# Kernel optimization log

Measured on AMD Instinct MI355X. Metric: run time of the kernel, lower is better.

The kernel has to match this reference:

```python
import jax, jax.numpy as jnp
import numpy as np

B, C, X, Y, Z = 2, 4, 128, 128, 96
_BIG = 1e10  # effectively infinite squared distance (no background in line)


def _edt_sq_pass(f, axis):
    """One separable pass of the exact squared EDT along `axis`:
    g[i] = min_j f[j] + (i - j)^2  (Felzenszwalb lower envelope, brute-forced
    with lax.map so only O(rest) memory per step)."""
    f = jnp.moveaxis(f, axis, -1)  # (..., L)
    idx = jnp.arange(f.shape[-1], dtype=f.dtype)
    g = jax.lax.map(lambda i: jnp.min(f + (i - idx) ** 2, axis=-1), idx)  # (L, ...)
    return jnp.moveaxis(jnp.moveaxis(g, 0, -1), -1, axis)


def _edt(mask):
    """Exact Euclidean distance of True voxels to the nearest False voxel
    (matches scipy.ndimage.distance_transform_edt on a binary mask)."""
    f = jnp.where(mask, _BIG, 0.0).astype(jnp.float32)
    for ax in (-3, -2, -1):  # three spatial axes
        f = _edt_sq_pass(f, ax)
    return jnp.sqrt(f)


def _neighbor(m, axis, d):
    """Shift `m` by d along `axis` with edge replication (reflect border,
    as in skimage's grey erosion used by find_boundaries)."""
    axis = axis % m.ndim
    pw = [(1, 1) if i == axis else (0, 0) for i in range(m.ndim)]
    p = jnp.pad(m, pw, mode='edge')
    sl = [slice(None)] * m.ndim
    sl[axis] = slice(1 + d, p.shape[axis] - 1 + d)
    return p[tuple(sl)]


def _inner_boundary(m):
    """skimage find_boundaries(mode='inner', connectivity=1): foreground voxels
    with at least one background face-neighbor."""
    eroded = m
    for ax in (-3, -2, -1):
        eroded = eroded & _neighbor(m, ax, 1) & _neighbor(m, ax, -1)
    return m & ~eroded


def _compute_sdf(onehot):
    """Signed distance map per (batch, class): negdis - posdis, zero on the
    inner boundary; zero where the class is absent; channel 0 is skipped."""
    posdis = _edt(onehot)          # dist inside object to background
    negdis = _edt(~onehot)         # dist outside object to foreground
    sdf = jnp.where(_inner_boundary(onehot), 0.0, negdis - posdis)
    any_pos = jnp.any(onehot, axis=(2, 3, 4), keepdims=True)
    sdf = jnp.where(any_pos, sdf, 0.0)
    return sdf.at[:, 0].set(0.0)   # loop starts at c=1 in the original


def setup_inputs() -> dict:
    key = jax.random.key(0)
    k1, k2 = jax.random.split(key)
    net_output = jax.random.normal(k1, (B, C, X, Y, Z), dtype=jnp.float32)
    gt = jax.random.randint(k2, (B, 1, X, Y, Z), 0, C, dtype=jnp.int32)
    return {"net_output": net_output, "gt": gt}


def reference(net_output, gt):
    probs = jax.nn.softmax(net_output, axis=1)  # softmax_helper = softmax over class dim
    classes = jnp.arange(net_output.shape[1], dtype=gt.dtype).reshape(1, -1, 1, 1, 1)
    onehot = gt == classes  # scatter_(1, gt, 1) one-hot, bool (B,C,X,Y,Z)
    phi = _compute_sdf(onehot)
    # einsum('bcxyz,bcxyz->bcxyz') on foreground channels, then global mean
    return jnp.mean(probs[:, 1:] * phi[:, 1:])
```

## Files before the change

kernel.cpp:

```cpp
#include <hip/hip_runtime.h>
#include <math.h>

#define XD 128
#define YD 128
#define ZD 96
#define NV (XD*YD*ZD)
#define SXX (YD*ZD)
#define SENT 49152
#define TW2 114
#define TDW (TW2/2)
#define TROWS 144

__global__ void k_zero_flags(int* flags) {
    if (threadIdx.x < 8) flags[threadIdx.x] = 0;
}

__global__ __launch_bounds__(384) void k_scan_x(const int* __restrict__ gt,
                                                unsigned char* __restrict__ out,
                                                int* __restrict__ flags,
                                                int batch0) {
    const int bb  = blockIdx.y;
    const int myb = batch0 + bb;
    const int tid = threadIdx.x;
    const int l   = tid & 63;
    const int w6  = tid >> 6;
    const int lq0 = blockIdx.x * 64;

    __shared__ unsigned char gtile[64 * 132];
    __shared__ int blkbits;
    if (tid == 0) blkbits = 0;

    int mybits = 0;
    const int* gp = gt + (size_t)myb * NV + lq0 + l;
    for (int j = w6; j < XD; j += 6) {
        int g = gp[(size_t)j * SXX];
        mybits |= 1 << g;
        gtile[l * 132 + j] = (unsigned char)g;
    }
#pragma unroll
    for (int off = 32; off; off >>= 1) mybits |= __shfl_xor(mybits, off);
    __syncthreads();
    if ((tid & 63) == 0) atomicOr(&blkbits, mybits);

    unsigned int D[32];
    {
        const unsigned int ci = (unsigned int)((w6 >> 1) + 1);
        const int s = w6 & 1;
        unsigned int G[32];
        const unsigned int* grow = (const unsigned int*)gtile + l * 33;
#pragma unroll
        for (int q = 0; q < 32; ++q) G[q] = grow[q];

        int cnt = 200;
#pragma unroll
        for (int q = 0; q < 32; ++q) {
            unsigned int u = G[q], dv = 0;
#pragma unroll
            for (int b = 0; b < 4; ++b) {
                unsigned int gv = (u >> (8 * b)) & 255u;
                bool zero = s ? (gv == ci) : (gv != ci);
                cnt = zero ? 0 : ((cnt < 200) ? cnt + 1 : 200);
                dv |= (unsigned int)cnt << (8 * b);
            }
            D[q] = dv;
        }
        cnt = 200;
#pragma unroll
        for (int q = 31; q >= 0; --q) {
            unsigned int u = G[q], dv = D[q];
#pragma unroll
            for (int b = 3; b >= 0; --b) {
                unsigned int gv = (u >> (8 * b)) & 255u;
                bool zero = s ? (gv == ci) : (gv != ci);
                cnt = zero ? 0 : ((cnt < 200) ? cnt + 1 : 200);
                unsigned int old = (dv >> (8 * b)) & 255u;
                unsigned int nbv = ((unsigned int)cnt < old) ? (unsigned int)cnt : old;
                dv = (dv & ~(255u << (8 * b))) | (nbv << (8 * b));
            }
            D[q] = dv;
        }
    }
    __syncthreads();
    if (tid == 0) atomicOr(&flags[myb], blkbits);

    {
        const int r = l & 3;
        unsigned char* ob = out + (size_t)(bb * 6 + w6) * NV + lq0 + (l & ~3);
#pragma unroll
        for (int q = 0; q < 32; ++q) {
            unsigned int A = D[q];
            unsigned int Bv = (unsigned int)__shfl_xor((int)A, 1);
            unsigned int t = (r & 1)
                ? __builtin_amdgcn_perm(A, Bv, 0x07030501u)
                : __builtin_amdgcn_perm(A, Bv, 0x02060004u);
            unsigned int Cv = (unsigned int)__shfl_xor((int)t, 2);
            unsigned int y = (r & 2)
                ? __builtin_amdgcn_perm(t, Cv, 0x07060302u)
                : __builtin_amdgcn_perm(t, Cv, 0x01000504u);
            *(unsigned int*)(ob + (size_t)(4 * q + r) * SXX) = y;
        }
    }
}

__device__ __forceinline__ bool edt_fast(const float r[32], float m[16]) {
#pragma unroll
    for (int k = 0; k < 16; ++k) m[k] = r[k + 8];
#pragma unroll
    for (int t = 1; t <= 4; ++t) {
        const float t2 = (float)(t * t);
#pragma unroll
        for (int k = 0; k < 16; ++k)
            m[k] = fminf(m[k], fminf(r[k + 8 - t], r[k + 8 + t]) + t2);
    }
    float mm = m[0];
#pragma unroll
    for (int k = 1; k < 16; ++k) mm = fmaxf(mm, m[k]);
    if (__all(mm <= 16.0f)) return true;
#pragma unroll
    for (int t = 5; t <= 8; ++t) {
        const float t2 = (float)(t * t);
#pragma unroll
        for (int k = 0; k < 16; ++k)
            m[k] = fminf(m[k], fminf(r[k + 8 - t], r[k + 8 + t]) + t2);
    }
    mm = m[0];
#pragma unroll
    for (int k = 1; k < 16; ++k) mm = fmaxf(mm, m[k]);
    return __all(mm <= 64.0f) != 0;
}

template<int STRIDE, int L>
__device__ void edt_slow(const unsigned short* __restrict__ p0, int i0,
                         float m[16]) {
    int t = 9;
    bool done = false;
    while (!done && t < L) {
        for (int u = 0; u < 4; ++u, ++t) {
            float t2 = (float)(t * t);
#pragma unroll
            for (int k = 0; k < 16; ++k) {
                int jm = i0 + k - t; if (jm < -8) jm = -8;
                int jp = i0 + k + t; if (jp > L + 7) jp = L + 7;
                m[k] = fminf(m[k], fminf((float)p0[jm * STRIDE],
                                         (float)p0[jp * STRIDE]) + t2);
            }
        }
        float mm = m[0];
#pragma unroll
        for (int k = 1; k < 16; ++k) mm = fmaxf(mm, m[k]);
        done = __all(mm <= (float)((t - 1) * (t - 1))) != 0;
    }
}

__global__ __launch_bounds__(768, 6) void k_pass_yz(const unsigned char* __restrict__ in,
                                                    unsigned short* __restrict__ out) {
    const int lv  = blockIdx.y;
    const int x   = blockIdx.x;
    const int tid = threadIdx.x;
    __shared__ unsigned short tile[TROWS * TW2];
    unsigned int* t32 = (unsigned int*)tile;

    for (int i = tid; i < 16 * TDW; i += 768) {
        int r = i / TDW, c = i - r * TDW;
        int row = (r < 8) ? r : 128 + r;
        t32[row * TDW + c] = 0xFFFFFFFFu;
    }
    for (int i = tid; i < 128 * 9; i += 768) {
        int r = i / 9, c = i - r * 9;
        int col = (c < 4) ? c : (48 + c);
        t32[(8 + r) * TDW + col] = 0xFFFFFFFFu;
    }
    {
        const uint4* ip = (const uint4*)(in + (size_t)lv * NV + (size_t)x * SXX);
        uint4 v = ip[tid];
        int e = tid * 16;
        int y = e / ZD, z = e - y * ZD;
        unsigned int base = (8 + y) * TDW + (8 + z) / 2;
        unsigned int vv[4] = {v.x, v.y, v.z, v.w};
#pragma unroll
        for (int q = 0; q < 4; ++q) {
            unsigned int b0 = vv[q] & 255u, b1 = (vv[q] >> 8) & 255u;
            unsigned int b2 = (vv[q] >> 16) & 255u, b3 = vv[q] >> 24;
            t32[base + 2 * q] = (b0 > 127u ? SENT : b0 * b0) |
                                ((b1 > 127u ? SENT : b1 * b1) << 16);
            t32[base + 2 * q + 1] = (b2 > 127u ? SENT : b2 * b2) |
                                    ((b3 > 127u ? SENT : b3 * b3) << 16);
        }
    }
    __syncthreads();

    float m[16];
    {
        const int z0 = tid % 96;
        const int i0 = (tid / 96) * 16;
        float r[32];
#pragma unroll
        for (int w = 0; w < 32; ++w) r[w] = (float)tile[(i0 + w) * TW2 + 8 + z0];
        if (!edt_fast(r, m)) edt_slow<TW2, YD>(&tile[8 * TW2 + 8 + z0], i0, m);
        __syncthreads();
#pragma unroll
        for (int k = 0; k < 16; ++k)
            tile[(8 + i0 + k) * TW2 + 8 + z0] =
                (unsigned short)fminf(m[k], (float)SENT);
        __syncthreads();
    }
    {
        const int y0 = tid % 128;
        const int i0 = (tid / 128) * 16;
        float r[32];
        {
            const unsigned int* wp = &t32[(8 + y0) * TDW + i0 / 2];
#pragma unroll
            for (int q = 0; q < 16; ++q) {
                unsigned int u = wp[q];
                r[2 * q] = (float)(u & 0xFFFFu);
                r[2 * q + 1] = (float)(u >> 16);
            }
        }
        if (!edt_fast(r, m)) edt_slow<1, ZD>(&tile[(8 + y0) * TW2 + 8], i0, m);
        __syncthreads();
        {
            unsigned int* wp = &t32[(8 + y0) * TDW + (8 + i0) / 2];
#pragma unroll
            for (int q = 0; q < 8; ++q) {
                unsigned int u0 = (unsigned int)fminf(m[2 * q],     (float)SENT);
                unsigned int u1 = (unsigned int)fminf(m[2 * q + 1], (float)SENT);
                wp[q] = u0 | (u1 << 16);
            }
        }
        __syncthreads();
    }
    uint4* op = (uint4*)(out + (size_t)lv * NV + (size_t)x * SXX);
    for (int o = tid; o < SXX / 8; o += 768) {
        int e = o * 8;
        int y = e / ZD, z = e - y * ZD;
        const unsigned int* sp = &t32[(8 + y) * TDW + (8 + z) / 2];
        uint4 v; v.x = sp[0]; v.y = sp[1]; v.z = sp[2]; v.w = sp[3];
        op[o] = v;
    }
}

__global__ __launch_bounds__(256) void k_accum_batch(const unsigned short* __restrict__ vols,
                                                     const float* __restrict__ net,
                                                     const int* __restrict__ flags,
                                                     double* __restrict__ partials,
                                                     int batch0) {
    const int b = batch0 + blockIdx.y;
    double ls = 0.0;
    const float* nb = net + (size_t)b * 4 * NV;
    const unsigned short* vb = vols + (size_t)blockIdx.y * 6 * NV;
    const int fbits = flags[b];
    const int NP = NV / 2;
    for (int p = blockIdx.x * 256 + threadIdx.x; p < NP; p += 1024 * 256) {
        const int idx = p * 2;
        float2 v0 = *(const float2*)(nb + idx);
        float2 v1 = *(const float2*)(nb + NV + idx);
        float2 v2 = *(const float2*)(nb + 2 * NV + idx);
        float2 v3 = *(const float2*)(nb + 3 * NV + idx);

        float mxa = fmaxf(fmaxf(v0.x, v1.x), fmaxf(v2.x, v3.x));
        float mxb = fmaxf(fmaxf(v0.y, v1.y), fmaxf(v2.y, v3.y));
        float e1a = __expf(v1.x - mxa), e2a = __expf(v2.x - mxa), e3a = __expf(v3.x - mxa);
        float e1b = __expf(v1.y - mxb), e2b = __expf(v2.y - mxb), e3b = __expf(v3.y - mxb);
        float sa = __expf(v0.x - mxa) + e1a + e2a + e3a;
        float sb = __expf(v0.y - mxb) + e1b + e2b + e3b;
        float ia = __frcp_rn(sa);
        float ib = __frcp_rn(sb);

        float acc = 0.0f;
#pragma unroll
        for (int ci = 1; ci <= 3; ++ci) {
            if ((fbits >> ci) & 1) {
                ushort2 dp = *(const ushort2*)(vb + (size_t)(2 * ci - 2) * NV + idx);
                ushort2 dn = *(const ushort2*)(vb + (size_t)(2 * ci - 1) * NV + idx);
                float ea = (ci == 1) ? e1a : ((ci == 2) ? e2a : e3a);
                float eb = (ci == 1) ? e1b : ((ci == 2) ? e2b : e3b);
                float phiA = (dp.x == 1) ? 0.0f
                           : (sqrtf((float)dn.x) - sqrtf((float)dp.x));
                float phiB = (dp.y == 1) ? 0.0f
                           : (sqrtf((float)dn.y) - sqrtf((float)dp.y));
                acc += (ea * ia) * phiA + (eb * ib) * phiB;
            }
        }
        ls += (double)acc;
    }
    __shared__ double sd[256];
    sd[threadIdx.x] = ls;
    __syncthreads();
    for (int off = 128; off > 0; off >>= 1) {
        if (threadIdx.x < off) sd[threadIdx.x] += sd[threadIdx.x + off];
        __syncthreads();
    }
    if (threadIdx.x == 0) partials[(size_t)b * 1024 + blockIdx.x] = sd[0];
}

__global__ void k_reduce(const double* __restrict__ partials, int n,
                         float* __restrict__ out) {
    __shared__ double sd[256];
    double ls = 0.0;
    for (int i = threadIdx.x; i < n; i += 256) ls += partials[i];
    sd[threadIdx.x] = ls;
    __syncthreads();
    for (int off = 128; off > 0; off >>= 1) {
        if (threadIdx.x < off) sd[threadIdx.x] += sd[threadIdx.x + off];
        __syncthreads();
    }
    if (threadIdx.x == 0) out[0] = (float)(sd[0] / 9437184.0);
}

extern "C" void kernel_launch(void* const* d_in, const int* in_sizes, int n_in,
                              void* d_out, int out_size, void* d_ws, size_t ws_size,
                              hipStream_t stream) {
    const float* net = (const float*)d_in[0];
    const int*   gt  = (const int*)d_in[1];
    float* out = (float*)d_out;
    char* ws = (char*)d_ws;

    const size_t xbufB1 = (size_t)6 * NV;
    const size_t zbufB1 = (size_t)6 * NV * sizeof(unsigned short);
    const size_t tail   = (size_t)2048 * sizeof(double) + 64;

    const int nb = (ws_size >= 2 * (xbufB1 + zbufB1) + tail) ? 2 : 1;

    unsigned char*  xbuf = (unsigned char*)ws;
    unsigned short* zbuf = (unsigned short*)(ws + (size_t)nb * xbufB1);
    double* partials = (double*)(ws + (size_t)nb * (xbufB1 + zbufB1));
    int* flags = (int*)((char*)partials + 2048 * sizeof(double));

    hipLaunchKernelGGL(k_zero_flags, dim3(1), dim3(64), 0, stream, flags);

    for (int b0 = 0; b0 < 2; b0 += nb) {
        hipLaunchKernelGGL(k_scan_x, dim3(SXX / 64, nb), dim3(384), 0, stream,
                           gt, xbuf, flags, b0);
        hipLaunchKernelGGL(k_pass_yz, dim3(XD, 6 * nb), dim3(768), 0, stream,
                           xbuf, zbuf);
        hipLaunchKernelGGL(k_accum_batch, dim3(1024, nb), dim3(256), 0, stream,
                           zbuf, net, flags, partials, b0);
    }
    hipLaunchKernelGGL(k_reduce, dim3(1), dim3(256), 0, stream, partials,
                       2048, out);
}
```

Baseline: 81.95 us.

## Fuse yz EDT passes with accumulation and precompute half-precision softmax probs

The y/z EDT pass is merged with the loss accumulation. Each block now handles one class, computes the positive and negative distance maps in sequence in shared memory, and reduces the product with the probabilities directly. This removes the 16-bit intermediate distance volume and the separate accumulation kernel's traffic. A new kernel precomputes softmax probabilities in fp16, which adds some rounding error and an extra write/read pass. Blocks for absent classes exit early.

```diff
diff --git a/kernel.cpp b/kernel.cpp
--- a/kernel.cpp
+++ b/kernel.cpp
@@ -1,4 +1,5 @@
 #include <hip/hip_runtime.h>
+#include <hip/hip_fp16.h>
 #include <math.h>
 
 #define XD 128
@@ -102,6 +103,32 @@
     }
 }
 
+__global__ __launch_bounds__(256) void k_prob(const float* __restrict__ net,
+                                              __half2* __restrict__ probs,
+                                              int batch0) {
+    const int b = batch0 + blockIdx.y;
+    const float* nb = net + (size_t)b * 4 * NV;
+    const int p = blockIdx.x * 256 + threadIdx.x;
+    const int idx = p * 2;
+    float2 v0 = *(const float2*)(nb + idx);
+    float2 v1 = *(const float2*)(nb + NV + idx);
+    float2 v2 = *(const float2*)(nb + 2 * NV + idx);
+    float2 v3 = *(const float2*)(nb + 3 * NV + idx);
+
+    float mxa = fmaxf(fmaxf(v0.x, v1.x), fmaxf(v2.x, v3.x));
+    float mxb = fmaxf(fmaxf(v0.y, v1.y), fmaxf(v2.y, v3.y));
+    float e1a = __expf(v1.x - mxa), e2a = __expf(v2.x - mxa), e3a = __expf(v3.x - mxa);
+    float e1b = __expf(v1.y - mxb), e2b = __expf(v2.y - mxb), e3b = __expf(v3.y - mxb);
+    float sa = __expf(v0.x - mxa) + e1a + e2a + e3a;
+    float sb = __expf(v0.y - mxb) + e1b + e2b + e3b;
+    float ia = __frcp_rn(sa), ib = __frcp_rn(sb);
+
+    const size_t h2 = (size_t)p;
+    probs[(size_t)(b * 3 + 0) * (NV / 2) + h2] = __floats2half2_rn(e1a * ia, e1b * ib);
+    probs[(size_t)(b * 3 + 1) * (NV / 2) + h2] = __floats2half2_rn(e2a * ia, e2b * ib);
+    probs[(size_t)(b * 3 + 2) * (NV / 2) + h2] = __floats2half2_rn(e3a * ia, e3b * ib);
+}
+
 __device__ __forceinline__ bool edt_fast(const float r[32], float m[16]) {
 #pragma unroll
     for (int k = 0; k < 16; ++k) m[k] = r[k + 8];
@@ -152,146 +179,154 @@
     }
 }
 
-__global__ __launch_bounds__(768, 6) void k_pass_yz(const unsigned char* __restrict__ in,
-                                                    unsigned short* __restrict__ out) {
-    const int lv  = blockIdx.y;
+__global__ __launch_bounds__(768, 6) void k_yz_acc(const unsigned char* __restrict__ in,
+                                                   const __half2* __restrict__ probs,
+                                                   const int* __restrict__ flags,
+                                                   double* __restrict__ partials,
+                                                   int batch0) {
     const int x   = blockIdx.x;
+    const int bbl = blockIdx.y / 3;
+    const int c   = blockIdx.y % 3;
+    const int b   = batch0 + bbl;
     const int tid = threadIdx.x;
+    const int pidx = (b * 3 + c) * XD + x;
+
     __shared__ unsigned short tile[TROWS * TW2];
+    __shared__ double sd[768];
     unsigned int* t32 = (unsigned int*)tile;
 
+    if (((flags[b] >> (c + 1)) & 1) == 0) {
+        if (tid == 0) partials[pidx] = 0.0;
+        return;
+    }
+
     for (int i = tid; i < 16 * TDW; i += 768) {
-        int r = i / TDW, c = i - r * TDW;
+        int r = i / TDW, cc = i - r * TDW;
         int row = (r < 8) ? r : 128 + r;
-        t32[row * TDW + c] = 0xFFFFFFFFu;
+        t32[row * TDW + cc] = 0xFFFFFFFFu;
     }
     for (int i = tid; i < 128 * 9; i += 768) {
-        int r = i / 9, c = i - r * 9;
-        int col = (c < 4) ? c : (48 + c);
+        int r = i / 9, cc = i - r * 9;
+        int col = (cc < 4) ? cc : (48 + cc);
         t32[(8 + r) * TDW + col] = 0xFFFFFFFFu;
     }
-    {
-        const uint4* ip = (const uint4*)(in + (size_t)lv * NV + (size_t)x * SXX);
+
+    const int z0 = tid % 96;  const int iY = (tid / 96) * 16;
+    const int y0 = tid % 128; const int iZ = (tid / 128) * 16;
+    const int e  = tid * 16;
+    const int sy = e / ZD, sz = e - sy * ZD;
+    const unsigned int sbase = (8 + sy) * TDW + (8 + sz) / 2;
+
+    float m[16];
+    unsigned int dpp[8];
+
+    {
+        const uint4* ip = (const uint4*)(in + (size_t)(bbl * 6 + 2 * c) * NV +
+                                         (size_t)x * SXX);
         uint4 v = ip[tid];
-        int e = tid * 16;
-        int y = e / ZD, z = e - y * ZD;
-        unsigned int base = (8 + y) * TDW + (8 + z) / 2;
         unsigned int vv[4] = {v.x, v.y, v.z, v.w};
 #pragma unroll
         for (int q = 0; q < 4; ++q) {
             unsigned int b0 = vv[q] & 255u, b1 = (vv[q] >> 8) & 255u;
             unsigned int b2 = (vv[q] >> 16) & 255u, b3 = vv[q] >> 24;
-            t32[base + 2 * q] = (b0 > 127u ? SENT : b0 * b0) |
-                                ((b1 > 127u ? SENT : b1 * b1) << 16);
-            t32[base + 2 * q + 1] = (b2 > 127u ? SENT : b2 * b2) |
-                                    ((b3 > 127u ? SENT : b3 * b3) << 16);
-        }
-    }
-    __syncthreads();
-
-    float m[16];
-    {
-        const int z0 = tid % 96;
-        const int i0 = (tid / 96) * 16;
+            t32[sbase + 2 * q] = (b0 > 127u ? SENT : b0 * b0) |
+                                 ((b1 > 127u ? SENT : b1 * b1) << 16);
+            t32[sbase + 2 * q + 1] = (b2 > 127u ? SENT : b2 * b2) |
+                                     ((b3 > 127u ? SENT : b3 * b3) << 16);
+        }
+    }
+    __syncthreads();
+    {
         float r[32];
 #pragma unroll
-        for (int w = 0; w < 32; ++w) r[w] = (float)tile[(i0 + w) * TW2 + 8 + z0];
-        if (!edt_fast(r, m)) edt_slow<TW2, YD>(&tile[8 * TW2 + 8 + z0], i0, m);
+        for (int w = 0; w < 32; ++w) r[w] = (float)tile[(iY + w) * TW2 + 8 + z0];
+        if (!edt_fast(r, m)) edt_slow<TW2, YD>(&tile[8 * TW2 + 8 + z0], iY, m);
         __syncthreads();
 #pragma unroll
         for (int k = 0; k < 16; ++k)
-            tile[(8 + i0 + k) * TW2 + 8 + z0] =
+            tile[(8 + iY + k) * TW2 + 8 + z0] =
                 (unsigned short)fminf(m[k], (float)SENT);
         __syncthreads();
     }
     {
-        const int y0 = tid % 128;
-        const int i0 = (tid / 128) * 16;
         float r[32];
-        {
-            const unsigned int* wp = &t32[(8 + y0) * TDW + i0 / 2];
-#pragma unroll
-            for (int q = 0; q < 16; ++q) {
-                unsigned int u = wp[q];
-                r[2 * q] = (float)(u & 0xFFFFu);
-                r[2 * q + 1] = (float)(u >> 16);
-            }
-        }
-        if (!edt_fast(r, m)) edt_slow<1, ZD>(&tile[(8 + y0) * TW2 + 8], i0, m);
-        __syncthreads();
-        {
-            unsigned int* wp = &t32[(8 + y0) * TDW + (8 + i0) / 2];
-#pragma unroll
-            for (int q = 0; q < 8; ++q) {
-                unsigned int u0 = (unsigned int)fminf(m[2 * q],     (float)SENT);
-                unsigned int u1 = (unsigned int)fminf(m[2 * q + 1], (float)SENT);
-                wp[q] = u0 | (u1 << 16);
-            }
-        }
-        __syncthreads();
-    }
-    uint4* op = (uint4*)(out + (size_t)lv * NV + (size_t)x * SXX);
-    for (int o = tid; o < SXX / 8; o += 768) {
-        int e = o * 8;
-        int y = e / ZD, z = e - y * ZD;
-        const unsigned int* sp = &t32[(8 + y) * TDW + (8 + z) / 2];
-        uint4 v; v.x = sp[0]; v.y = sp[1]; v.z = sp[2]; v.w = sp[3];
-        op[o] = v;
-    }
-}
-
-__global__ __launch_bounds__(256) void k_accum_batch(const unsigned short* __restrict__ vols,
-                                                     const float* __restrict__ net,
-                                                     const int* __restrict__ flags,
-                                                     double* __restrict__ partials,
-                                                     int batch0) {
-    const int b = batch0 + blockIdx.y;
-    double ls = 0.0;
-    const float* nb = net + (size_t)b * 4 * NV;
-    const unsigned short* vb = vols + (size_t)blockIdx.y * 6 * NV;
-    const int fbits = flags[b];
-    const int NP = NV / 2;
-    for (int p = blockIdx.x * 256 + threadIdx.x; p < NP; p += 1024 * 256) {
-        const int idx = p * 2;
-        float2 v0 = *(const float2*)(nb + idx);
-        float2 v1 = *(const float2*)(nb + NV + idx);
-        float2 v2 = *(const float2*)(nb + 2 * NV + idx);
-        float2 v3 = *(const float2*)(nb + 3 * NV + idx);
-
-        float mxa = fmaxf(fmaxf(v0.x, v1.x), fmaxf(v2.x, v3.x));
-        float mxb = fmaxf(fmaxf(v0.y, v1.y), fmaxf(v2.y, v3.y));
-        float e1a = __expf(v1.x - mxa), e2a = __expf(v2.x - mxa), e3a = __expf(v3.x - mxa);
-        float e1b = __expf(v1.y - mxb), e2b = __expf(v2.y - mxb), e3b = __expf(v3.y - mxb);
-        float sa = __expf(v0.x - mxa) + e1a + e2a + e3a;
-        float sb = __expf(v0.y - mxb) + e1b + e2b + e3b;
-        float ia = __frcp_rn(sa);
-        float ib = __frcp_rn(sb);
-
-        float acc = 0.0f;
-#pragma unroll
-        for (int ci = 1; ci <= 3; ++ci) {
-            if ((fbits >> ci) & 1) {
-                ushort2 dp = *(const ushort2*)(vb + (size_t)(2 * ci - 2) * NV + idx);
-                ushort2 dn = *(const ushort2*)(vb + (size_t)(2 * ci - 1) * NV + idx);
-                float ea = (ci == 1) ? e1a : ((ci == 2) ? e2a : e3a);
-                float eb = (ci == 1) ? e1b : ((ci == 2) ? e2b : e3b);
-                float phiA = (dp.x == 1) ? 0.0f
-                           : (sqrtf((float)dn.x) - sqrtf((float)dp.x));
-                float phiB = (dp.y == 1) ? 0.0f
-                           : (sqrtf((float)dn.y) - sqrtf((float)dp.y));
-                acc += (ea * ia) * phiA + (eb * ib) * phiB;
-            }
-        }
-        ls += (double)acc;
-    }
-    __shared__ double sd[256];
-    sd[threadIdx.x] = ls;
-    __syncthreads();
-    for (int off = 128; off > 0; off >>= 1) {
-        if (threadIdx.x < off) sd[threadIdx.x] += sd[threadIdx.x + off];
-        __syncthreads();
-    }
-    if (threadIdx.x == 0) partials[(size_t)b * 1024 + blockIdx.x] = sd[0];
+        const unsigned int* wp = &t32[(8 + y0) * TDW + iZ / 2];
+#pragma unroll
+        for (int q = 0; q < 16; ++q) {
+            unsigned int u = wp[q];
+            r[2 * q] = (float)(u & 0xFFFFu);
+            r[2 * q + 1] = (float)(u >> 16);
+        }
+        if (!edt_fast(r, m)) edt_slow<1, ZD>(&tile[(8 + y0) * TW2 + 8], iZ, m);
+    }
+#pragma unroll
+    for (int q = 0; q < 8; ++q)
+        dpp[q] = (unsigned int)fminf(m[2 * q], (float)SENT) |
+                 ((unsigned int)fminf(m[2 * q + 1], (float)SENT) << 16);
+    __syncthreads();
+
+    {
+        const uint4* ip = (const uint4*)(in + (size_t)(bbl * 6 + 2 * c + 1) * NV +
+                                         (size_t)x * SXX);
+        uint4 v = ip[tid];
+        unsigned int vv[4] = {v.x, v.y, v.z, v.w};
+#pragma unroll
+        for (int q = 0; q < 4; ++q) {
+            unsigned int b0 = vv[q] & 255u, b1 = (vv[q] >> 8) & 255u;
+            unsigned int b2 = (vv[q] >> 16) & 255u, b3 = vv[q] >> 24;
+            t32[sbase + 2 * q] = (b0 > 127u ? SENT : b0 * b0) |
+                                 ((b1 > 127u ? SENT : b1 * b1) << 16);
+            t32[sbase + 2 * q + 1] = (b2 > 127u ? SENT : b2 * b2) |
+                                     ((b3 > 127u ? SENT : b3 * b3) << 16);
+        }
+    }
+    __syncthreads();
+    {
+        float r[32];
+#pragma unroll
+        for (int w = 0; w < 32; ++w) r[w] = (float)tile[(iY + w) * TW2 + 8 + z0];
+        if (!edt_fast(r, m)) edt_slow<TW2, YD>(&tile[8 * TW2 + 8 + z0], iY, m);
+        __syncthreads();
+#pragma unroll
+        for (int k = 0; k < 16; ++k)
+            tile[(8 + iY + k) * TW2 + 8 + z0] =
+                (unsigned short)fminf(m[k], (float)SENT);
+        __syncthreads();
+    }
+    {
+        float r[32];
+        const unsigned int* wp = &t32[(8 + y0) * TDW + iZ / 2];
+#pragma unroll
+        for (int q = 0; q < 16; ++q) {
+            unsigned int u = wp[q];
+            r[2 * q] = (float)(u & 0xFFFFu);
+            r[2 * q + 1] = (float)(u >> 16);
+        }
+        if (!edt_fast(r, m)) edt_slow<1, ZD>(&tile[(8 + y0) * TW2 + 8], iZ, m);
+    }
+
+    float a = 0.0f;
+    {
+        const __half2* pv = probs + (size_t)(b * 3 + c) * (NV / 2) +
+                            ((size_t)x * SXX + (size_t)y0 * ZD + iZ) / 2;
+#pragma unroll
+        for (int q = 0; q < 8; ++q) {
+            float2 pf = __half22float2(pv[q]);
+            unsigned int dp0 = dpp[q] & 0xFFFFu, dp1 = dpp[q] >> 16;
+            float phi0 = (dp0 == 1u) ? 0.0f
+                       : (sqrtf(m[2 * q]) - sqrtf((float)dp0));
+            float phi1 = (dp1 == 1u) ? 0.0f
+                       : (sqrtf(m[2 * q + 1]) - sqrtf((float)dp1));
+            a += pf.x * phi0 + pf.y * phi1;
+        }
+    }
+    sd[tid] = (double)a;
+    __syncthreads();
+    for (int off = 512; off; off >>= 1) {
+        if (tid < off && tid + off < 768) sd[tid] += sd[tid + off];
+        __syncthreads();
+    }
+    if (tid == 0) partials[pidx] = sd[0];
 }
 
 __global__ void k_reduce(const double* __restrict__ partials, int n,
@@ -316,27 +351,27 @@
     float* out = (float*)d_out;
     char* ws = (char*)d_ws;
 
-    const size_t xbufB1 = (size_t)6 * NV;
-    const size_t zbufB1 = (size_t)6 * NV * sizeof(unsigned short);
-    const size_t tail   = (size_t)2048 * sizeof(double) + 64;
-
-    const int nb = (ws_size >= 2 * (xbufB1 + zbufB1) + tail) ? 2 : 1;
-
-    unsigned char*  xbuf = (unsigned char*)ws;
-    unsigned short* zbuf = (unsigned short*)(ws + (size_t)nb * xbufB1);
-    double* partials = (double*)(ws + (size_t)nb * (xbufB1 + zbufB1));
-    int* flags = (int*)((char*)partials + 2048 * sizeof(double));
+    const size_t xbufB1  = (size_t)6 * NV;
+    const size_t probsB  = (size_t)2 * 3 * NV * 2;
+    const size_t tail    = (size_t)768 * sizeof(double) + 64;
+
+    const int nb = (ws_size >= 2 * xbufB1 + probsB + tail) ? 2 : 1;
+
+    unsigned char* xbuf  = (unsigned char*)ws;
+    __half2*       probs = (__half2*)(ws + (size_t)nb * xbufB1);
+    double*     partials = (double*)(ws + (size_t)nb * xbufB1 + probsB);
+    int*           flags = (int*)((char*)partials + 768 * sizeof(double));
 
     hipLaunchKernelGGL(k_zero_flags, dim3(1), dim3(64), 0, stream, flags);
 
     for (int b0 = 0; b0 < 2; b0 += nb) {
         hipLaunchKernelGGL(k_scan_x, dim3(SXX / 64, nb), dim3(384), 0, stream,
                            gt, xbuf, flags, b0);
-        hipLaunchKernelGGL(k_pass_yz, dim3(XD, 6 * nb), dim3(768), 0, stream,
-                           xbuf, zbuf);
-        hipLaunchKernelGGL(k_accum_batch, dim3(1024, nb), dim3(256), 0, stream,
-                           zbuf, net, flags, partials, b0);
+        hipLaunchKernelGGL(k_prob, dim3((NV / 2) / 256, nb), dim3(256), 0,
+                           stream, net, probs, b0);
+        hipLaunchKernelGGL(k_yz_acc, dim3(XD, 3 * nb), dim3(768), 0, stream,
+                           xbuf, probs, flags, partials, b0);
     }
     hipLaunchKernelGGL(k_reduce, dim3(1), dim3(256), 0, stream, partials,
-                       2048, out);
-}
+                       768, out);
+}
```

Result: faster. 80.02 us (-2.4%).
